# Optimization experiments

Measured on AMD Instinct MI355X. Metric: run time of the kernel, lower is better.

## Reference

```python
import jax, jax.numpy as jnp
import numpy as np

T, B, D = 2048, 16, 1024

def setup_inputs() -> dict:
    key = jax.random.key(0)
    k1, k2 = jax.random.split(key)
    x = jax.random.normal(k1, (T, B, D), dtype=jnp.float32)
    # xavier-uniform init for W (dim, dim)
    limit = float(np.sqrt(6.0 / (D + D)))
    W = jax.random.uniform(k2, (D, D), dtype=jnp.float32, minval=-limit, maxval=limit)
    b = jnp.zeros((D,), dtype=jnp.float32)
    return {"x": x, "W": W, "b": b}

def reference(x, W, b):
    Tn, Bn, Dn = x.shape
    h0 = jnp.zeros((Bn, Dn), dtype=x.dtype)
    # parallel projection: v_t = W @ x_t + b for all t
    proj_all = jnp.einsum('tbd,ed->tbe', x, W) + b  # [T, B, D]

    def step(h_prev, proj):
        alpha = jax.nn.sigmoid(proj)
        h_new = alpha * h_prev + (1.0 - alpha) * jnp.tanh(proj)
        out = h_new * jax.nn.silu(h_new)  # h * silu(h)
        return h_new, (h_new, out)

    _, (hs, outputs) = jax.lax.scan(step, h0, proj_all)
    h = jnp.concatenate([h0[None], hs], axis=0)  # [T+1, B, D]
    return (outputs, h)
```

## Files before the change

kernel.cpp:

```cpp
#include <hip/hip_runtime.h>

#define T_DIM 2048
#define B_DIM 16
#define D_DIM 1024
#define M_DIM (T_DIM * B_DIM)
#define K_DIM D_DIM
#define N_DIM D_DIM
#define BD    (B_DIM * D_DIM)
#define NCH   32
#define CHL   (T_DIM / NCH)
#define NQ    (BD / 4)

typedef _Float16 f16;
typedef __attribute__((ext_vector_type(8)))  _Float16 f16x8;
typedef __attribute__((ext_vector_type(4)))  float    f32x4;

#define GLD16(g, l) __builtin_amdgcn_global_load_lds(                        \
    (const __attribute__((address_space(1))) unsigned*)(g),                  \
    (__attribute__((address_space(3))) unsigned*)(l), 16, 0, 0)

#define BARRIER do { asm volatile("" ::: "memory");                          \
                     __builtin_amdgcn_s_barrier();                           \
                     asm volatile("" ::: "memory"); } while (0)

__device__ __forceinline__ void stepAB(float p, float& A, float& B) {
    const float ep  = __expf(-p);
    const float al  = __builtin_amdgcn_rcpf(1.f + ep);
    const float be  = ep * al;
    const float ep2 = ep * ep;
    const float th  = (1.f - ep2) * __builtin_amdgcn_rcpf(1.f + ep2);
    A = A * al;
    B = fmaf(al, B, be * th);
}
__device__ __forceinline__ void stepH(float p, float& h) {
    const float ep  = __expf(-p);
    const float al  = __builtin_amdgcn_rcpf(1.f + ep);
    const float be  = ep * al;
    const float ep2 = ep * ep;
    const float th  = (1.f - ep2) * __builtin_amdgcn_rcpf(1.f + ep2);
    h = fmaf(al, h, be * th);
}
__device__ __forceinline__ float outOf(float h) {
    const float sh = __builtin_amdgcn_rcpf(1.f + __expf(-h));
    return h * h * sh;
}


__global__ __launch_bounds__(256) void convert_x(const float* __restrict__ x,
                                                 ushort* __restrict__ Xf) {
    __shared__ ushort tile[4096];
    const int b   = (int)blockIdx.x;
    const int br  = b >> 5;
    const int kt  = b & 31;
    const int tid = (int)threadIdx.x;
#pragma unroll
    for (int i = 0; i < 4; ++i) {
        const int fi  = tid + i * 256;
        const int row = fi >> 3;
        const int kq  = fi & 7;
        const float4 v = *(const float4*)&x[(size_t)(br * 128 + row) * K_DIM + kt * 32 + kq * 4];
        ushort4 u;
        u.x = __builtin_bit_cast(unsigned short, (f16)v.x);
        u.y = __builtin_bit_cast(unsigned short, (f16)v.y);
        u.z = __builtin_bit_cast(unsigned short, (f16)v.z);
        u.w = __builtin_bit_cast(unsigned short, (f16)v.w);
        const int idx = ((kq >> 1) * 128 + row) * 8 + (kq & 1) * 4;
        *(ushort4*)&tile[idx] = u;
    }
    __syncthreads();
    const uint4* s = (const uint4*)tile;
    uint4* d = (uint4*)(Xf + (size_t)b * 4096);
    d[tid] = s[tid];
    d[tid + 256] = s[tid + 256];
}

__global__ __launch_bounds__(256) void convert_w(const float* __restrict__ W,
                                                 ushort* __restrict__ Wh) {
    __shared__ ushort th[4096];
    const int b   = (int)blockIdx.x;
    const int bc  = b >> 5;
    const int kt  = b & 31;
    const int tid = (int)threadIdx.x;
#pragma unroll
    for (int i = 0; i < 4; ++i) {
        const int fi  = tid + i * 256;
        const int col = fi >> 3;
        const int kq  = fi & 7;
        const float4 v = *(const float4*)&W[(size_t)(bc * 128 + col) * K_DIM + kt * 32 + kq * 4];
        ushort4 u;
        u.x = __builtin_bit_cast(unsigned short, (f16)v.x);
        u.y = __builtin_bit_cast(unsigned short, (f16)v.y);
        u.z = __builtin_bit_cast(unsigned short, (f16)v.z);
        u.w = __builtin_bit_cast(unsigned short, (f16)v.w);
        const int idx = ((kq >> 1) * 128 + col) * 8 + (kq & 1) * 4;
        *(ushort4*)&th[idx] = u;
    }
    __syncthreads();
    const uint4* s = (const uint4*)th;
    uint4* d = (uint4*)(Wh + (size_t)b * 4096);
    d[tid] = s[tid];
    d[tid + 256] = s[tid + 256];
}

template <int OUT16>
__global__ __launch_bounds__(256, 4) void gemm_proj(const ushort* __restrict__ Xf,
                                                    const ushort* __restrict__ Wh,
                                                    const float* __restrict__ bias,
                                                    float* __restrict__ proj32,
                                                    ushort* __restrict__ proj16) {
    __shared__ ushort sA[2][4096];
    __shared__ ushort sB[2][4096];

    const int bid = (int)blockIdx.x;
    const int swz = (bid & 7) * 256 + (bid >> 3);
    const int bc  = swz & 7;
    const int br  = swz >> 3;
    const int tid  = (int)threadIdx.x;
    const int lane = tid & 63;
    const int wid  = tid >> 6;
    const int wr = (wid >> 1) * 64;
    const int wc = (wid & 1) * 64;
    const int l16 = lane & 15;
    const int lc  = lane >> 4;

    const char* aG = (const char*)(Xf + (size_t)br * 32 * 4096);
    const char* bG = (const char*)(Wh + (size_t)bc * 32 * 4096);

    f32x4 acc[4][4];
#pragma unroll
    for (int m = 0; m < 4; ++m)
#pragma unroll
        for (int n = 0; n < 4; ++n)
#pragma unroll
            for (int r = 0; r < 4; ++r) acc[m][n][r] = 0.f;

#define STAGE(t, buf) do {                                                   \
        const size_t tb = (size_t)(t) * 8192;                                \
        GLD16(aG + tb + tid * 16,        (char*)&sA[buf][0] + tid * 16);     \
        GLD16(aG + tb + tid * 16 + 4096, (char*)&sA[buf][0] + tid * 16 + 4096); \
        GLD16(bG + tb + tid * 16,        (char*)&sB[buf][0] + tid * 16);     \
        GLD16(bG + tb + tid * 16 + 4096, (char*)&sB[buf][0] + tid * 16 + 4096); \
    } while (0)

    STAGE(0, 0);
    STAGE(1, 1);

    for (int t = 0; t < 32; ++t) {
        if (t < 31) asm volatile("s_waitcnt vmcnt(4)" ::: "memory");
        else        asm volatile("s_waitcnt vmcnt(0)" ::: "memory");
        BARRIER;
        const int cur = t & 1;
        {
            const int ab = (lc * 128 + wr + l16) * 8;
            const int bb = (lc * 128 + wc + l16) * 8;
            f16x8 fa[4], fb[4];
#pragma unroll
            for (int m = 0; m < 4; ++m)
                fa[m] = *(const f16x8*)&sA[cur][ab + m * 128];
#pragma unroll
            for (int n = 0; n < 4; ++n)
                fb[n] = *(const f16x8*)&sB[cur][bb + n * 128];
#pragma unroll
            for (int m = 0; m < 4; ++m)
#pragma unroll
                for (int n = 0; n < 4; ++n)
                    acc[m][n] = __builtin_amdgcn_mfma_f32_16x16x32_f16(fa[m], fb[n], acc[m][n], 0, 0, 0);
        }
        BARRIER;
        if (t < 30) STAGE(t + 2, cur);
    }
#undef STAGE

#pragma unroll
    for (int n = 0; n < 4; ++n) {
        const int colg = bc * 128 + wc + n * 16 + l16;
        const float bz = bias[colg];
#pragma unroll
        for (int m = 0; m < 4; ++m) {
            const int rowg = br * 128 + wr + m * 16 + lc * 4;
#pragma unroll
            for (int r = 0; r < 4; ++r) {
                const float v = acc[m][n][r] + bz;
                if constexpr (OUT16)
                    proj16[(size_t)(rowg + r) * N_DIM + colg] =
                        __builtin_bit_cast(unsigned short, (f16)v);
                else
                    proj32[(size_t)(rowg + r) * N_DIM + colg] = v;
            }
        }
    }
}

__global__ __launch_bounds__(256) void scan_pass1h(const ushort* __restrict__ po,
                                                   float* __restrict__ Ac,
                                                   float* __restrict__ Bc) {
    const int blk = (int)blockIdx.x;
    const int c   = blk >> 3;
    const int q   = (blk & 7) * 256 + (int)threadIdx.x;
    const ushort* pp = po + (size_t)c * CHL * BD + (size_t)q * 8;

    float A[8], B[8];
#pragma unroll
    for (int e = 0; e < 8; ++e) { A[e] = 1.f; B[e] = 0.f; }

    f16x8 cur[4], nxt[4];
#pragma unroll
    for (int j = 0; j < 4; ++j) cur[j] = *(const f16x8*)&pp[(size_t)j * BD];
    for (int g = 0; g < CHL / 4; ++g) {
        if (g + 1 < CHL / 4) {
#pragma unroll
            for (int j = 0; j < 4; ++j)
                nxt[j] = *(const f16x8*)&pp[(size_t)((g + 1) * 4 + j) * BD];
        }
#pragma unroll
        for (int j = 0; j < 4; ++j)
#pragma unroll
            for (int e = 0; e < 8; ++e)
                stepAB((float)cur[j][e], A[e], B[e]);
#pragma unroll
        for (int j = 0; j < 4; ++j) cur[j] = nxt[j];
    }
    float* ap = Ac + (size_t)c * BD + (size_t)q * 8;
    float* bp = Bc + (size_t)c * BD + (size_t)q * 8;
    *(float4*)&ap[0] = make_float4(A[0], A[1], A[2], A[3]);
    *(float4*)&ap[4] = make_float4(A[4], A[5], A[6], A[7]);
    *(float4*)&bp[0] = make_float4(B[0], B[1], B[2], B[3]);
    *(float4*)&bp[4] = make_float4(B[4], B[5], B[6], B[7]);
}

__global__ __launch_bounds__(256) void scan_pass2h(const ushort* __restrict__ po,
                                                   const float* __restrict__ Ac,
                                                   const float* __restrict__ Bc,
                                                   float* __restrict__ out,
                                                   float* __restrict__ h_out) {
    const int blk = (int)blockIdx.x;
    const int c   = blk >> 3;
    const int q   = (blk & 7) * 256 + (int)threadIdx.x;

    float h[8];
#pragma unroll
    for (int e = 0; e < 8; ++e) h[e] = 0.f;
    for (int j = 0; j < c; ++j) {
        const float* ap = Ac + (size_t)j * BD + (size_t)q * 8;
        const float* bp = Bc + (size_t)j * BD + (size_t)q * 8;
        const float4 a0 = *(const float4*)&ap[0], a1 = *(const float4*)&ap[4];
        const float4 b0 = *(const float4*)&bp[0], b1 = *(const float4*)&bp[4];
        h[0] = fmaf(a0.x, h[0], b0.x); h[1] = fmaf(a0.y, h[1], b0.y);
        h[2] = fmaf(a0.z, h[2], b0.z); h[3] = fmaf(a0.w, h[3], b0.w);
        h[4] = fmaf(a1.x, h[4], b1.x); h[5] = fmaf(a1.y, h[5], b1.y);
        h[6] = fmaf(a1.z, h[6], b1.z); h[7] = fmaf(a1.w, h[7], b1.w);
    }
    if (c == 0) {
        *(float4*)&h_out[(size_t)q * 8]     = make_float4(0.f, 0.f, 0.f, 0.f);
        *(float4*)&h_out[(size_t)q * 8 + 4] = make_float4(0.f, 0.f, 0.f, 0.f);
    }

    const ushort* pp = po + (size_t)c * CHL * BD + (size_t)q * 8;
    float* op = out   + (size_t)c * CHL * BD + (size_t)q * 8;
    float* hp = h_out + (size_t)c * CHL * BD + (size_t)q * 8 + BD;

    f16x8 cur[4], nxt[4];
#pragma unroll
    for (int j = 0; j < 4; ++j) cur[j] = *(const f16x8*)&pp[(size_t)j * BD];
    for (int g = 0; g < CHL / 4; ++g) {
        if (g + 1 < CHL / 4) {
#pragma unroll
            for (int j = 0; j < 4; ++j)
                nxt[j] = *(const f16x8*)&pp[(size_t)((g + 1) * 4 + j) * BD];
        }
#pragma unroll
        for (int j = 0; j < 4; ++j) {
            const size_t so = (size_t)(g * 4 + j) * BD;
            float o[8];
#pragma unroll
            for (int e = 0; e < 8; ++e) {
                stepH((float)cur[j][e], h[e]);
                o[e] = outOf(h[e]);
            }
            *(float4*)&op[so]     = make_float4(o[0], o[1], o[2], o[3]);
            *(float4*)&op[so + 4] = make_float4(o[4], o[5], o[6], o[7]);
            *(float4*)&hp[so]     = make_float4(h[0], h[1], h[2], h[3]);
            *(float4*)&hp[so + 4] = make_float4(h[4], h[5], h[6], h[7]);
        }
#pragma unroll
        for (int j = 0; j < 4; ++j) cur[j] = nxt[j];
    }
}

__global__ __launch_bounds__(256) void scan_pass1(const float* __restrict__ po,
                                                  float4* __restrict__ Ac,
                                                  float4* __restrict__ Bc) {
    const int blk = (int)blockIdx.x;
    const int c   = blk >> 4;
    const int q   = (blk & 15) * 256 + (int)threadIdx.x;
    const float* pp = po + (size_t)c * CHL * BD + (size_t)q * 4;

    float4 A = make_float4(1.f, 1.f, 1.f, 1.f);
    float4 B = make_float4(0.f, 0.f, 0.f, 0.f);
    float4 cur[4], nxt[4];
#pragma unroll
    for (int j = 0; j < 4; ++j) cur[j] = *(const float4*)&pp[(size_t)j * BD];
    for (int g = 0; g < CHL / 4; ++g) {
        if (g + 1 < CHL / 4) {
#pragma unroll
            for (int j = 0; j < 4; ++j)
                nxt[j] = *(const float4*)&pp[(size_t)((g + 1) * 4 + j) * BD];
        }
#pragma unroll
        for (int j = 0; j < 4; ++j) {
            stepAB(cur[j].x, A.x, B.x);
            stepAB(cur[j].y, A.y, B.y);
            stepAB(cur[j].z, A.z, B.z);
            stepAB(cur[j].w, A.w, B.w);
        }
#pragma unroll
        for (int j = 0; j < 4; ++j) cur[j] = nxt[j];
    }
    Ac[c * NQ + q] = A;
    Bc[c * NQ + q] = B;
}

__global__ __launch_bounds__(256) void scan_pass2(float* __restrict__ po,
                                                  const float4* __restrict__ Ac,
                                                  const float4* __restrict__ Bc,
                                                  float* __restrict__ h_out) {
    const int blk = (int)blockIdx.x;
    const int c   = blk >> 4;
    const int q   = (blk & 15) * 256 + (int)threadIdx.x;

    float4 h = make_float4(0.f, 0.f, 0.f, 0.f);
    for (int j = 0; j < c; ++j) {
        const float4 A = Ac[j * NQ + q];
        const float4 B = Bc[j * NQ + q];
        h.x = fmaf(A.x, h.x, B.x);
        h.y = fmaf(A.y, h.y, B.y);
        h.z = fmaf(A.z, h.z, B.z);
        h.w = fmaf(A.w, h.w, B.w);
    }
    if (c == 0) *(float4*)&h_out[(size_t)q * 4] = make_float4(0.f, 0.f, 0.f, 0.f);

    float* pp = po + (size_t)c * CHL * BD + (size_t)q * 4;
    float* hp = h_out + (size_t)c * CHL * BD + (size_t)q * 4 + BD;

    float4 cur[4], nxt[4];
#pragma unroll
    for (int j = 0; j < 4; ++j) cur[j] = *(const float4*)&pp[(size_t)j * BD];
    for (int g = 0; g < CHL / 4; ++g) {
        if (g + 1 < CHL / 4) {
#pragma unroll
            for (int j = 0; j < 4; ++j)
                nxt[j] = *(const float4*)&pp[(size_t)((g + 1) * 4 + j) * BD];
        }
#pragma unroll
        for (int j = 0; j < 4; ++j) {
            const size_t so = (size_t)(g * 4 + j) * BD;
            stepH(cur[j].x, h.x);
            stepH(cur[j].y, h.y);
            stepH(cur[j].z, h.z);
            stepH(cur[j].w, h.w);
            float4 o;
            o.x = outOf(h.x); o.y = outOf(h.y); o.z = outOf(h.z); o.w = outOf(h.w);
            *(float4*)&pp[so] = o;
            *(float4*)&hp[so] = h;
        }
#pragma unroll
        for (int j = 0; j < 4; ++j) cur[j] = nxt[j];
    }
}

__global__ __launch_bounds__(64) void scan_fused(float* __restrict__ po,
                                                 float* __restrict__ h_out) {
    const int idx = (int)blockIdx.x * 64 + (int)threadIdx.x;
    float h = 0.f;
    h_out[idx] = 0.f;
    size_t off = (size_t)idx;
#pragma unroll 4
    for (int t = 0; t < T_DIM; ++t) {
        float p = po[off];
        stepH(p, h);
        po[off] = outOf(h);
        h_out[off + BD] = h;
        off += BD;
    }
}

extern "C" void kernel_launch(void* const* d_in, const int* in_sizes, int n_in,
                              void* d_out, int out_size, void* d_ws, size_t ws_size,
                              hipStream_t stream) {
    const float* x = (const float*)d_in[0];
    const float* W = (const float*)d_in[1];
    const float* b = (const float*)d_in[2];
    float* out = (float*)d_out;
    float* h   = out + (size_t)T_DIM * B_DIM * D_DIM;

    ushort* Xf = (ushort*)h;
    ushort* Wh = Xf + (size_t)M_DIM * K_DIM;

    convert_x<<<8192, 256, 0, stream>>>(x, Xf);
    convert_w<<<256, 256, 0, stream>>>(W, Wh);

    const size_t P16_BYTES = (size_t)M_DIM * N_DIM * 2;
    const size_t AB_BYTES  = (size_t)NCH * BD * 4;

    if (ws_size >= P16_BYTES + 2 * AB_BYTES) {
        ushort* P16 = (ushort*)d_ws;
        float*  Ac  = (float*)((char*)d_ws + P16_BYTES);
        float*  Bc  = Ac + (size_t)NCH * BD;
        gemm_proj<1><<<2048, 256, 0, stream>>>(Xf, Wh, b, nullptr, P16);
        scan_pass1h<<<(NCH - 1) * 8, 256, 0, stream>>>(P16, Ac, Bc);
        scan_pass2h<<<NCH * 8, 256, 0, stream>>>(P16, Ac, Bc, out, h);
    } else if (ws_size >= (size_t)4 * 1024 * 1024) {
        float4* Ac = (float4*)d_ws;
        float4* Bc = Ac + (size_t)NCH * NQ;
        gemm_proj<0><<<2048, 256, 0, stream>>>(Xf, Wh, b, out, nullptr);
        scan_pass1<<<(NCH - 1) * 16, 256, 0, stream>>>(out, Ac, Bc);
        scan_pass2<<<NCH * 16, 256, 0, stream>>>(out, Ac, Bc, h);
    } else {
        gemm_proj<0><<<2048, 256, 0, stream>>>(Xf, Wh, b, out, nullptr);
        scan_fused<<<BD / 64, 64, 0, stream>>>(out, h);
    }
}
```

Baseline: 221.1 us.

## Enlarge GEMM tiles to 256x256 with 8 waves and phased prefetch pipeline

The projection GEMM moves from 128x128 tiles with 4 waves to 256x256 tiles with 8 waves per block and a K-step of 64. Each K-step is split into four phases that interleave global-to-LDS prefetch of the next buffer with MFMA work, and s_setprio raises wave priority during the MFMA bursts. The two conversion kernels are merged into one that writes the matching 256-row, 64-wide K tile layout. The goal is more operand reuse per LDS load and better overlap of loads with compute, at the cost of 128KB of LDS per block, only one block per CU, and 512 blocks in total, which may not balance evenly across the CUs.

```diff
diff --git a/kernel.cpp b/kernel.cpp
--- a/kernel.cpp
+++ b/kernel.cpp
@@ -46,141 +46,154 @@
 }
 
 
-__global__ __launch_bounds__(256) void convert_x(const float* __restrict__ x,
-                                                 ushort* __restrict__ Xf) {
-    __shared__ ushort tile[4096];
+__global__ __launch_bounds__(256) void convert_tiles(const float* __restrict__ src,
+                                                     ushort* __restrict__ dst) {
+    __shared__ ushort tile[16384];
     const int b   = (int)blockIdx.x;
-    const int br  = b >> 5;
-    const int kt  = b & 31;
+    const int sr  = b >> 4;
+    const int kt  = b & 15;
     const int tid = (int)threadIdx.x;
 #pragma unroll
-    for (int i = 0; i < 4; ++i) {
+    for (int i = 0; i < 16; ++i) {
         const int fi  = tid + i * 256;
-        const int row = fi >> 3;
-        const int kq  = fi & 7;
-        const float4 v = *(const float4*)&x[(size_t)(br * 128 + row) * K_DIM + kt * 32 + kq * 4];
+        const int row = fi >> 4;
+        const int kq  = fi & 15;
+        const float4 v = *(const float4*)&src[(size_t)(sr * 256 + row) * K_DIM + kt * 64 + kq * 4];
         ushort4 u;
         u.x = __builtin_bit_cast(unsigned short, (f16)v.x);
         u.y = __builtin_bit_cast(unsigned short, (f16)v.y);
         u.z = __builtin_bit_cast(unsigned short, (f16)v.z);
         u.w = __builtin_bit_cast(unsigned short, (f16)v.w);
-        const int idx = ((kq >> 1) * 128 + row) * 8 + (kq & 1) * 4;
+        const int idx = ((kq >> 1) * 256 + row) * 8 + (kq & 1) * 4;
         *(ushort4*)&tile[idx] = u;
     }
     __syncthreads();
     const uint4* s = (const uint4*)tile;
-    uint4* d = (uint4*)(Xf + (size_t)b * 4096);
-    d[tid] = s[tid];
-    d[tid + 256] = s[tid + 256];
-}
-
-__global__ __launch_bounds__(256) void convert_w(const float* __restrict__ W,
-                                                 ushort* __restrict__ Wh) {
-    __shared__ ushort th[4096];
-    const int b   = (int)blockIdx.x;
-    const int bc  = b >> 5;
-    const int kt  = b & 31;
-    const int tid = (int)threadIdx.x;
-#pragma unroll
-    for (int i = 0; i < 4; ++i) {
-        const int fi  = tid + i * 256;
-        const int col = fi >> 3;
-        const int kq  = fi & 7;
-        const float4 v = *(const float4*)&W[(size_t)(bc * 128 + col) * K_DIM + kt * 32 + kq * 4];
-        ushort4 u;
-        u.x = __builtin_bit_cast(unsigned short, (f16)v.x);
-        u.y = __builtin_bit_cast(unsigned short, (f16)v.y);
-        u.z = __builtin_bit_cast(unsigned short, (f16)v.z);
-        u.w = __builtin_bit_cast(unsigned short, (f16)v.w);
-        const int idx = ((kq >> 1) * 128 + col) * 8 + (kq & 1) * 4;
-        *(ushort4*)&th[idx] = u;
-    }
-    __syncthreads();
-    const uint4* s = (const uint4*)th;
-    uint4* d = (uint4*)(Wh + (size_t)b * 4096);
-    d[tid] = s[tid];
-    d[tid + 256] = s[tid + 256];
+    uint4* d = (uint4*)(dst + (size_t)b * 16384);
+#pragma unroll
+    for (int i = 0; i < 8; ++i) d[tid + i * 256] = s[tid + i * 256];
 }
 
 template <int OUT16>
-__global__ __launch_bounds__(256, 4) void gemm_proj(const ushort* __restrict__ Xf,
+__global__ __launch_bounds__(512, 1) void gemm_proj(const ushort* __restrict__ Xf,
                                                     const ushort* __restrict__ Wh,
                                                     const float* __restrict__ bias,
                                                     float* __restrict__ proj32,
                                                     ushort* __restrict__ proj16) {
-    __shared__ ushort sA[2][4096];
-    __shared__ ushort sB[2][4096];
+    __shared__ ushort sA[2][16384];
+    __shared__ ushort sB[2][16384];
 
     const int bid = (int)blockIdx.x;
-    const int swz = (bid & 7) * 256 + (bid >> 3);
-    const int bc  = swz & 7;
-    const int br  = swz >> 3;
+    const int swz = (bid & 7) * 64 + (bid >> 3);
+    const int bc  = swz & 3;
+    const int br  = swz >> 2;
     const int tid  = (int)threadIdx.x;
     const int lane = tid & 63;
     const int wid  = tid >> 6;
-    const int wr = (wid >> 1) * 64;
-    const int wc = (wid & 1) * 64;
+    const int wr = (wid >> 2) * 128;
+    const int wc = (wid & 3) * 64;
     const int l16 = lane & 15;
-    const int lc  = lane >> 4;
-
-    const char* aG = (const char*)(Xf + (size_t)br * 32 * 4096);
-    const char* bG = (const char*)(Wh + (size_t)bc * 32 * 4096);
-
-    f32x4 acc[4][4];
-#pragma unroll
-    for (int m = 0; m < 4; ++m)
+    const int lc  = (lane >> 4) & 3;
+
+    const char* aG = (const char*)(Xf + (size_t)br * 16 * 16384);
+    const char* bG = (const char*)(Wh + (size_t)bc * 16 * 16384);
+
+    float bz[4];
+#pragma unroll
+    for (int n = 0; n < 4; ++n)
+        bz[n] = bias[bc * 256 + wc + n * 16 + l16];
+    asm volatile("s_waitcnt vmcnt(0)" ::: "memory");
+
+    f32x4 acc[8][4];
+#pragma unroll
+    for (int m = 0; m < 8; ++m)
 #pragma unroll
         for (int n = 0; n < 4; ++n)
 #pragma unroll
             for (int r = 0; r < 4; ++r) acc[m][n][r] = 0.f;
 
-#define STAGE(t, buf) do {                                                   \
-        const size_t tb = (size_t)(t) * 8192;                                \
-        GLD16(aG + tb + tid * 16,        (char*)&sA[buf][0] + tid * 16);     \
-        GLD16(aG + tb + tid * 16 + 4096, (char*)&sA[buf][0] + tid * 16 + 4096); \
-        GLD16(bG + tb + tid * 16,        (char*)&sB[buf][0] + tid * 16);     \
-        GLD16(bG + tb + tid * 16 + 4096, (char*)&sB[buf][0] + tid * 16 + 4096); \
+#define STG_A0(ST, SB_) do { const size_t tb_ = (size_t)(ST) * 32768;        \
+        GLD16(aG + tb_ + tid * 16,        (char*)&sA[SB_][0] + tid * 16);    \
+        GLD16(aG + tb_ + tid * 16 + 8192, (char*)&sA[SB_][0] + tid * 16 + 8192); } while (0)
+#define STG_B0(ST, SB_) do { const size_t tb_ = (size_t)(ST) * 32768;        \
+        GLD16(bG + tb_ + tid * 16,        (char*)&sB[SB_][0] + tid * 16);    \
+        GLD16(bG + tb_ + tid * 16 + 8192, (char*)&sB[SB_][0] + tid * 16 + 8192); } while (0)
+#define STG_A1(ST, SB_) do { const size_t tb_ = (size_t)(ST) * 32768;        \
+        GLD16(aG + tb_ + tid * 16 + 16384, (char*)&sA[SB_][0] + tid * 16 + 16384); \
+        GLD16(aG + tb_ + tid * 16 + 24576, (char*)&sA[SB_][0] + tid * 16 + 24576); } while (0)
+#define STG_B1(ST, SB_) do { const size_t tb_ = (size_t)(ST) * 32768;        \
+        GLD16(bG + tb_ + tid * 16 + 16384, (char*)&sB[SB_][0] + tid * 16 + 16384); \
+        GLD16(bG + tb_ + tid * 16 + 24576, (char*)&sB[SB_][0] + tid * 16 + 24576); } while (0)
+
+#define FENCE4 asm volatile("s_waitcnt vmcnt(4)" ::: "memory")
+#define FENCE8 asm volatile("s_waitcnt vmcnt(8)" ::: "memory")
+#define FENCE0 asm volatile("s_waitcnt vmcnt(0)" ::: "memory")
+
+#define PHASE(BUF, KC, MG, STAGE_STMT, FENCE_STMT) do {                      \
+        f16x8 fa[4], fb[4];                                                  \
+        _Pragma("unroll")                                                    \
+        for (int mm = 0; mm < 4; ++mm)                                       \
+            fa[mm] = *(const f16x8*)&sA[BUF][(((KC)*4 + lc) * 256 + wr + ((MG)*4 + mm) * 16 + l16) * 8]; \
+        _Pragma("unroll")                                                    \
+        for (int nn = 0; nn < 4; ++nn)                                       \
+            fb[nn] = *(const f16x8*)&sB[BUF][(((KC)*4 + lc) * 256 + wc + nn * 16 + l16) * 8]; \
+        STAGE_STMT;                                                          \
+        FENCE_STMT;                                                          \
+        BARRIER;                                                             \
+        __builtin_amdgcn_s_setprio(1);                                       \
+        _Pragma("unroll")                                                    \
+        for (int mm = 0; mm < 4; ++mm)                                       \
+            _Pragma("unroll")                                                \
+            for (int nn = 0; nn < 4; ++nn)                                   \
+                acc[(MG)*4 + mm][nn] = __builtin_amdgcn_mfma_f32_16x16x32_f16( \
+                    fa[mm], fb[nn], acc[(MG)*4 + mm][nn], 0, 0, 0);          \
+        __builtin_amdgcn_s_setprio(0);                                       \
+        BARRIER;                                                             \
     } while (0)
 
-    STAGE(0, 0);
-    STAGE(1, 1);
-
-    for (int t = 0; t < 32; ++t) {
-        if (t < 31) asm volatile("s_waitcnt vmcnt(4)" ::: "memory");
-        else        asm volatile("s_waitcnt vmcnt(0)" ::: "memory");
-        BARRIER;
-        const int cur = t & 1;
-        {
-            const int ab = (lc * 128 + wr + l16) * 8;
-            const int bb = (lc * 128 + wc + l16) * 8;
-            f16x8 fa[4], fb[4];
-#pragma unroll
-            for (int m = 0; m < 4; ++m)
-                fa[m] = *(const f16x8*)&sA[cur][ab + m * 128];
-#pragma unroll
-            for (int n = 0; n < 4; ++n)
-                fb[n] = *(const f16x8*)&sB[cur][bb + n * 128];
-#pragma unroll
-            for (int m = 0; m < 4; ++m)
-#pragma unroll
-                for (int n = 0; n < 4; ++n)
-                    acc[m][n] = __builtin_amdgcn_mfma_f32_16x16x32_f16(fa[m], fb[n], acc[m][n], 0, 0, 0);
-        }
-        BARRIER;
-        if (t < 30) STAGE(t + 2, cur);
-    }
-#undef STAGE
+    STG_A0(0, 0); STG_B0(0, 0); STG_A1(0, 0); STG_B1(0, 0);
+    STG_A0(1, 1); STG_B0(1, 1); STG_A1(1, 1); STG_B1(1, 1);
+    FENCE4;
+    BARRIER;
+
+    PHASE(0, 0, 0, , );
+    PHASE(0, 0, 1, , );
+    PHASE(0, 1, 0, , );
+    PHASE(0, 1, 1, , );
+
+    for (int u = 0; u < 7; ++u) {
+        const int t1 = 2 * u + 2;
+        const int t2 = 2 * u + 3;
+        PHASE(1, 0, 0, STG_A0(t1, 0), );
+        PHASE(1, 0, 1, STG_B0(t1, 0), FENCE4);
+        PHASE(1, 1, 0, STG_A1(t1, 0), );
+        PHASE(1, 1, 1, STG_B1(t1, 0), FENCE4);
+        PHASE(0, 0, 0, STG_A0(t2, 1), );
+        PHASE(0, 0, 1, STG_B0(t2, 1), FENCE4);
+        PHASE(0, 1, 0, STG_A1(t2, 1), );
+        PHASE(0, 1, 1, STG_B1(t2, 1), FENCE4);
+    }
+
+    PHASE(1, 0, 0, , );
+    PHASE(1, 0, 1, , FENCE0);
+    PHASE(1, 1, 0, , );
+    PHASE(1, 1, 1, , );
+
+#undef PHASE
+#undef STG_A0
+#undef STG_B0
+#undef STG_A1
+#undef STG_B1
 
 #pragma unroll
     for (int n = 0; n < 4; ++n) {
-        const int colg = bc * 128 + wc + n * 16 + l16;
-        const float bz = bias[colg];
-#pragma unroll
-        for (int m = 0; m < 4; ++m) {
-            const int rowg = br * 128 + wr + m * 16 + lc * 4;
+        const int colg = bc * 256 + wc + n * 16 + l16;
+#pragma unroll
+        for (int m = 0; m < 8; ++m) {
+            const int rowg = br * 256 + wr + m * 16 + lc * 4;
 #pragma unroll
             for (int r = 0; r < 4; ++r) {
-                const float v = acc[m][n][r] + bz;
+                const float v = acc[m][n][r] + bz[n];
                 if constexpr (OUT16)
                     proj16[(size_t)(rowg + r) * N_DIM + colg] =
                         __builtin_bit_cast(unsigned short, (f16)v);
@@ -396,8 +409,8 @@
     ushort* Xf = (ushort*)h;
     ushort* Wh = Xf + (size_t)M_DIM * K_DIM;
 
-    convert_x<<<8192, 256, 0, stream>>>(x, Xf);
-    convert_w<<<256, 256, 0, stream>>>(W, Wh);
+    convert_tiles<<<2048, 256, 0, stream>>>(x, Xf);
+    convert_tiles<<<64, 256, 0, stream>>>(W, Wh);
 
     const size_t P16_BYTES = (size_t)M_DIM * N_DIM * 2;
     const size_t AB_BYTES  = (size_t)NCH * BD * 4;
@@ -406,17 +419,17 @@
         ushort* P16 = (ushort*)d_ws;
         float*  Ac  = (float*)((char*)d_ws + P16_BYTES);
         float*  Bc  = Ac + (size_t)NCH * BD;
-        gemm_proj<1><<<2048, 256, 0, stream>>>(Xf, Wh, b, nullptr, P16);
+        gemm_proj<1><<<512, 512, 0, stream>>>(Xf, Wh, b, nullptr, P16);
         scan_pass1h<<<(NCH - 1) * 8, 256, 0, stream>>>(P16, Ac, Bc);
         scan_pass2h<<<NCH * 8, 256, 0, stream>>>(P16, Ac, Bc, out, h);
     } else if (ws_size >= (size_t)4 * 1024 * 1024) {
         float4* Ac = (float4*)d_ws;
         float4* Bc = Ac + (size_t)NCH * NQ;
-        gemm_proj<0><<<2048, 256, 0, stream>>>(Xf, Wh, b, out, nullptr);
+        gemm_proj<0><<<512, 512, 0, stream>>>(Xf, Wh, b, out, nullptr);
         scan_pass1<<<(NCH - 1) * 16, 256, 0, stream>>>(out, Ac, Bc);
         scan_pass2<<<NCH * 16, 256, 0, stream>>>(out, Ac, Bc, h);
     } else {
-        gemm_proj<0><<<2048, 256, 0, stream>>>(Xf, Wh, b, out, nullptr);
+        gemm_proj<0><<<512, 512, 0, stream>>>(Xf, Wh, b, out, nullptr);
         scan_fused<<<BD / 64, 64, 0, stream>>>(out, h);
     }
 }
```

Result: no change. 218.1 us (-1.3%).
